# Performance work log

Hardware: AMD Instinct MI355X
Metric: run time of the kernel (lower is better)

## Reference

```python
import jax, jax.numpy as jnp
import numpy as np

EPS = 1e-5


def _layernorm(x, w, b):
    mu = jnp.mean(x, axis=-1, keepdims=True)
    var = jnp.var(x, axis=-1, keepdims=True)
    return (x - mu) * jax.lax.rsqrt(var + EPS) * w + b


def setup_inputs() -> dict:
    key = jax.random.key(0)
    ks = jax.random.split(key, 5)
    B, I, H = 8192, 1024, 1024
    inp = {
        "input": jax.random.normal(ks[0], (B, I), dtype=jnp.float32),
        "hx": jax.random.normal(ks[1], (B, H), dtype=jnp.float32),
        "cx": jax.random.normal(ks[2], (B, H), dtype=jnp.float32),
        # parameters (torch initializes weights with randn; LN weight=1, bias=0)
        "weight_ih": jax.random.normal(ks[3], (4 * H, I), dtype=jnp.float32),
        "weight_hh": jax.random.normal(ks[4], (4 * H, H), dtype=jnp.float32),
        "ln_i_w": jnp.ones((4 * H,), jnp.float32),
        "ln_i_b": jnp.zeros((4 * H,), jnp.float32),
        "ln_h_w": jnp.ones((4 * H,), jnp.float32),
        "ln_h_b": jnp.zeros((4 * H,), jnp.float32),
        "ln_c_w": jnp.ones((H,), jnp.float32),
        "ln_c_b": jnp.zeros((H,), jnp.float32),
    }
    return inp


def reference(input, hx, cx, weight_ih, weight_hh,
              ln_i_w, ln_i_b, ln_h_w, ln_h_b, ln_c_w, ln_c_b):
    # gate pre-activations: [B, 4H]
    igates = _layernorm(input @ weight_ih.T, ln_i_w, ln_i_b)
    hgates = _layernorm(hx @ weight_hh.T, ln_h_w, ln_h_b)
    gates = igates + hgates
    ingate, forgetgate, cellgate, outgate = jnp.split(gates, 4, axis=-1)
    ingate = jax.nn.sigmoid(ingate)
    forgetgate = jax.nn.sigmoid(forgetgate)
    cellgate = jnp.tanh(cellgate)
    outgate = jax.nn.sigmoid(outgate)
    cy = _layernorm(forgetgate * cx + ingate * cellgate, ln_c_w, ln_c_b)
    hy = outgate * jnp.tanh(cy)  # activation=Tanh, dropout p=0 is identity
    return (hy, cy)
```

## Files before the change

### kernel.cpp

```cpp
#include <hip/hip_runtime.h>
#include <hip/hip_bf16.h>
#include <cstdint>
#include <cstddef>

typedef __bf16 bf16_t;
typedef bf16_t bf16x8 __attribute__((ext_vector_type(8)));
typedef float floatx4 __attribute__((ext_vector_type(4)));

static constexpr int B_ = 8192;
static constexpr int H_ = 1024;
static constexpr int G4 = 4096;
static constexpr int K_ = 1024;

__device__ inline void async_copy16(const bf16_t* g, bf16_t* l) {
  auto l3 = (__attribute__((address_space(3))) void*)(uint32_t)(uintptr_t)l;
  __builtin_amdgcn_global_load_lds(
      (__attribute__((address_space(1))) void*)(uintptr_t)g, l3, 16, 0, 0);
}

__global__ __launch_bounds__(256) void prep_all(
    const float* __restrict__ input, const float* __restrict__ hx,
    const float* __restrict__ wih, const float* __restrict__ whh,
    bf16_t* __restrict__ Abf, bf16_t* __restrict__ Hbf,
    bf16_t* __restrict__ Wib, bf16_t* __restrict__ Whb) {
  const int bid = blockIdx.x;
  if (bid < 4096) {
    const int nt = B_ * K_ / 16;
    int gid = bid * 256 + threadIdx.x;
    const float* src; bf16_t* dst; int idx;
    if (gid < nt) { src = input; dst = Abf; idx = gid; }
    else          { src = hx;    dst = Hbf; idx = gid - nt; }
    const float4* s4 = (const float4*)src + (size_t)idx * 4;
    const float4 v0 = s4[0], v1 = s4[1], v2 = s4[2], v3 = s4[3];
    bf16x8 o0, o1;
    o0[0] = (bf16_t)v0.x; o0[1] = (bf16_t)v0.y; o0[2] = (bf16_t)v0.z; o0[3] = (bf16_t)v0.w;
    o0[4] = (bf16_t)v1.x; o0[5] = (bf16_t)v1.y; o0[6] = (bf16_t)v1.z; o0[7] = (bf16_t)v1.w;
    o1[0] = (bf16_t)v2.x; o1[1] = (bf16_t)v2.y; o1[2] = (bf16_t)v2.z; o1[3] = (bf16_t)v2.w;
    o1[4] = (bf16_t)v3.x; o1[5] = (bf16_t)v3.y; o1[6] = (bf16_t)v3.z; o1[7] = (bf16_t)v3.w;
    ((bf16x8*)dst)[(size_t)idx * 2]     = o0;
    ((bf16x8*)dst)[(size_t)idx * 2 + 1] = o1;
  } else {
    const int r  = bid - 4096;
    const int rr = r * 2 + (threadIdx.x >> 7);
    const int rp = rr & 4095;
    const float* src = (rr < 4096) ? wih : whh;
    bf16_t*      dst = (rr < 4096) ? Wib : Whb;
    const int h = rp >> 2, g = rp & 3;
    const int rin = g * 1024 + h;
    const int c = (threadIdx.x & 127) * 8;
    const float4 v0 = *(const float4*)(src + (size_t)rin * K_ + c);
    const float4 v1 = *(const float4*)(src + (size_t)rin * K_ + c + 4);
    bf16x8 o;
    o[0] = (bf16_t)v0.x; o[1] = (bf16_t)v0.y; o[2] = (bf16_t)v0.z; o[3] = (bf16_t)v0.w;
    o[4] = (bf16_t)v1.x; o[5] = (bf16_t)v1.y; o[6] = (bf16_t)v1.z; o[7] = (bf16_t)v1.w;
    *(bf16x8*)(dst + (size_t)rp * K_ + c) = o;
  }
}


#define FENCE() asm volatile("" ::: "memory")
#define BARRIER() do { FENCE(); __builtin_amdgcn_s_barrier(); FENCE(); } while (0)

__global__ __launch_bounds__(512, 2) void gemm_bt8(
    const bf16_t* __restrict__ A, const bf16_t* __restrict__ W,
    bf16_t* __restrict__ C) {
  constexpr int N = G4, K = K_, NT = K_ / 64;

  __shared__ bf16_t ldsA[2][16384];
  __shared__ bf16_t ldsB[2][16384];

  const int flatb = blockIdx.x + (blockIdx.y << 4);
  const int swzb  = (flatb & 7) * 64 + (flatb >> 3);
  const int by = swzb >> 4;
  const int bx = swzb & 15;

  const int tid  = threadIdx.x;
  const int lane = tid & 63;
  const int w    = tid >> 6;
  const int wm   = w >> 2, wn = w & 3;
  const int lrow = lane & 15, quad = lane >> 4;
  const int e    = lrow & 7;

  const int m0 = by * 256;
  const int n0 = bx * 256;

  const int srow   = tid >> 3;
  const int schunk = (tid & 7) ^ (srow & 7);
  const bf16_t* gA = A + (size_t)(m0 + srow) * K + schunk * 8;
  const bf16_t* gB = W + (size_t)(n0 + srow) * K + schunk * 8;
  const int wslot = w * 512;

  const int aBase = (wm * 128 + lrow) * 64 + (quad ^ e) * 8;
  const int bBase = (wn * 64 + lrow) * 64 + (quad ^ e) * 8;

  floatx4 acc[8][4] = {};
  bf16x8 aF[4][2];
  bf16x8 bF[2][2][2];

#define STG_A(p, half, kt) do {                                          \
    bf16_t* _l = &ldsA[p][(half) * 8192 + wslot];                        \
    async_copy16(gA + (size_t)((half) * 128) * K + (kt) * 64, _l);       \
    async_copy16(gA + (size_t)((half) * 128 + 64) * K + (kt) * 64, _l + 4096); \
  } while (0)
#define STG_B(p, half, kt) do {                                          \
    bf16_t* _l = &ldsB[p][(half) * 8192 + wslot];                        \
    async_copy16(gB + (size_t)((half) * 128) * K + (kt) * 64, _l);       \
    async_copy16(gB + (size_t)((half) * 128 + 64) * K + (kt) * 64, _l + 4096); \
  } while (0)

#define LD_A(p, qm) do { _Pragma("unroll")                               \
    for (int i2 = 0; i2 < 4; ++i2) {                                     \
      const int o = aBase + (qm) * 4096 + i2 * 1024;                     \
      aF[i2][0] = *(const bf16x8*)&ldsA[p][o];                           \
      aF[i2][1] = *(const bf16x8*)&ldsA[p][o ^ 32];                      \
    } } while (0)
#define LD_B(p, qn) do { _Pragma("unroll")                               \
    for (int j2 = 0; j2 < 2; ++j2) {                                     \
      const int o = bBase + (qn) * 2048 + j2 * 1024;                     \
      bF[qn][j2][0] = *(const bf16x8*)&ldsB[p][o];                       \
      bF[qn][j2][1] = *(const bf16x8*)&ldsB[p][o ^ 32];                  \
    } } while (0)
#define MFMA_Q(qm, qn) do { _Pragma("unroll")                            \
    for (int i2 = 0; i2 < 4; ++i2) { _Pragma("unroll")                   \
      for (int j2 = 0; j2 < 2; ++j2) {                                   \
        floatx4& c = acc[(qm) * 4 + i2][(qn) * 2 + j2];                  \
        c = __builtin_amdgcn_mfma_f32_16x16x32_bf16(aF[i2][0], bF[qn][j2][0], c, 0, 0, 0); \
        c = __builtin_amdgcn_mfma_f32_16x16x32_bf16(aF[i2][1], bF[qn][j2][1], c, 0, 0, 0); \
      } } } while (0)

  STG_B(0, 0, 0); STG_B(0, 1, 0);
  STG_A(0, 0, 0); STG_A(0, 1, 0);
  STG_B(1, 0, 1); STG_B(1, 1, 1);
  asm volatile("s_waitcnt vmcnt(4)" ::: "memory");
  BARRIER();

#pragma unroll 2
  for (int t = 0; t < NT; ++t) {
    const int p = t & 1, q = p ^ 1;
    const int t1 = (t + 1) & (NT - 1), t2 = (t + 2) & (NT - 1);

    LD_A(p, 0); LD_B(p, 0);
    STG_A(q, 0, t1);
    BARRIER();
    asm volatile("s_waitcnt lgkmcnt(0)" ::: "memory");
    __builtin_amdgcn_sched_barrier(0);
    __builtin_amdgcn_s_setprio(1); MFMA_Q(0, 0); __builtin_amdgcn_s_setprio(0);
    BARRIER();

    LD_B(p, 1);
    STG_A(q, 1, t1);
    BARRIER();
    asm volatile("s_waitcnt lgkmcnt(0)" ::: "memory");
    __builtin_amdgcn_sched_barrier(0);
    __builtin_amdgcn_s_setprio(1); MFMA_Q(0, 1); __builtin_amdgcn_s_setprio(0);
    BARRIER();

    LD_A(p, 1);
    STG_B(p, 0, t2);
    BARRIER();
    asm volatile("s_waitcnt lgkmcnt(0)" ::: "memory");
    __builtin_amdgcn_sched_barrier(0);
    __builtin_amdgcn_s_setprio(1); MFMA_Q(1, 0); __builtin_amdgcn_s_setprio(0);
    BARRIER();

    STG_B(p, 1, t2);
    BARRIER();
    __builtin_amdgcn_s_setprio(1); MFMA_Q(1, 1); __builtin_amdgcn_s_setprio(0);
    asm volatile("s_waitcnt vmcnt(4)" ::: "memory");
    BARRIER();
  }

#pragma unroll
  for (int i = 0; i < 8; ++i) {
    const int mbase = m0 + wm * 128 + i * 16 + quad * 4;
#pragma unroll
    for (int j = 0; j < 4; ++j) {
      const int n = n0 + wn * 64 + j * 16 + lrow;
#pragma unroll
      for (int r = 0; r < 4; ++r)
        C[(size_t)(mbase + r) * N + n] = (bf16_t)acc[i][j][r];
    }
  }
#undef STG_A
#undef STG_B
#undef LD_A
#undef LD_B
#undef MFMA_Q
}

__device__ inline float sigmoid_f(float x) { return 1.0f / (1.0f + __expf(-x)); }
__device__ inline float tanh_f(float x) {
  float e = __expf(2.0f * x);
  return 1.0f - 2.0f / (e + 1.0f);
}

__global__ __launch_bounds__(256) void ln_lstm_epi_wave2(
    const bf16_t* __restrict__ IG, const bf16_t* __restrict__ HG,
    const float* __restrict__ cx,
    const float* __restrict__ wi, const float* __restrict__ bi,
    const float* __restrict__ wh, const float* __restrict__ bh,
    const float* __restrict__ wc, const float* __restrict__ bc,
    float* __restrict__ hy_out, float* __restrict__ cy_out) {
  const int l = threadIdx.x & 63;
  const int b = blockIdx.x * 4 + (threadIdx.x >> 6);

  const bf16_t* igp = IG + (size_t)b * 4096;
  const bf16_t* hgp = HG + (size_t)b * 4096;

  bf16x8 igv[4][2], hgv[4][2];
  float4 cx4[4];
#pragma unroll
  for (int c = 0; c < 4; ++c) {
    const int n0 = c * 1024 + l * 16;
    igv[c][0] = *(const bf16x8*)(igp + n0);
    igv[c][1] = *(const bf16x8*)(igp + n0 + 8);
    hgv[c][0] = *(const bf16x8*)(hgp + n0);
    hgv[c][1] = *(const bf16x8*)(hgp + n0 + 8);
    cx4[c] = *(const float4*)(cx + (size_t)b * 1024 + c * 256 + l * 4);
  }

  float si = 0, qi = 0, sh = 0, qh = 0;
#pragma unroll
  for (int c = 0; c < 4; ++c)
#pragma unroll
    for (int hf = 0; hf < 2; ++hf)
#pragma unroll
      for (int e = 0; e < 8; ++e) {
        const float a = (float)igv[c][hf][e], d = (float)hgv[c][hf][e];
        si += a; qi = fmaf(a, a, qi);
        sh += d; qh = fmaf(d, d, qh);
      }
#pragma unroll
  for (int off = 1; off < 64; off <<= 1) {
    si += __shfl_xor(si, off); qi += __shfl_xor(qi, off);
    sh += __shfl_xor(sh, off); qh += __shfl_xor(qh, off);
  }
  const float invN = 1.0f / 4096.0f;
  const float mui = si * invN, muh = sh * invN;
  const float rsi = rsqrtf(fmaxf(qi * invN - mui * mui, 0.0f) + 1e-5f);
  const float rsh = rsqrtf(fmaxf(qh * invN - muh * muh, 0.0f) + 1e-5f);

  float cv[16], ov[16];
  float sc = 0, qc = 0;
#pragma unroll
  for (int c = 0; c < 4; ++c) {
    const int h0 = c * 256 + l * 4;
    float4 wiv[4], biv[4], whv[4], bhv[4];
#pragma unroll
    for (int g = 0; g < 4; ++g) {
      wiv[g] = *(const float4*)(wi + g * 1024 + h0);
      biv[g] = *(const float4*)(bi + g * 1024 + h0);
      whv[g] = *(const float4*)(wh + g * 1024 + h0);
      bhv[g] = *(const float4*)(bh + g * 1024 + h0);
    }
#pragma unroll
    for (int k = 0; k < 4; ++k) {
      float G[4];
#pragma unroll
      for (int g = 0; g < 4; ++g) {
        const int idx = k * 4 + g;
        const float gi = (float)igv[c][idx >> 3][idx & 7];
        const float gh = (float)hgv[c][idx >> 3][idx & 7];
        G[g] = (gi - mui) * rsi * ((const float*)&wiv[g])[k] + ((const float*)&biv[g])[k] +
               (gh - muh) * rsh * ((const float*)&whv[g])[k] + ((const float*)&bhv[g])[k];
      }
      const float in_g = sigmoid_f(G[0]);
      const float fo_g = sigmoid_f(G[1]);
      const float ce_g = tanh_f(G[2]);
      ov[c * 4 + k] = sigmoid_f(G[3]);
      const float cc = fo_g * ((const float*)&cx4[c])[k] + in_g * ce_g;
      cv[c * 4 + k] = cc;
      sc += cc; qc = fmaf(cc, cc, qc);
    }
  }
#pragma unroll
  for (int off = 1; off < 64; off <<= 1) {
    sc += __shfl_xor(sc, off); qc += __shfl_xor(qc, off);
  }
  const float invH = 1.0f / 1024.0f;
  const float muc = sc * invH;
  const float rsc = rsqrtf(fmaxf(qc * invH - muc * muc, 0.0f) + 1e-5f);

#pragma unroll
  for (int c = 0; c < 4; ++c) {
    const int h0 = c * 256 + l * 4;
    const float4 wc4 = *(const float4*)(wc + h0);
    const float4 bc4 = *(const float4*)(bc + h0);
    float4 cyv, hyv;
#pragma unroll
    for (int k = 0; k < 4; ++k) {
      const float cyn = (cv[c * 4 + k] - muc) * rsc * ((const float*)&wc4)[k] +
                        ((const float*)&bc4)[k];
      ((float*)&cyv)[k] = cyn;
      ((float*)&hyv)[k] = ov[c * 4 + k] * tanh_f(cyn);
    }
    *(float4*)(cy_out + (size_t)b * 1024 + h0) = cyv;
    *(float4*)(hy_out + (size_t)b * 1024 + h0) = hyv;
  }
}

extern "C" void kernel_launch(void* const* d_in, const int* in_sizes, int n_in,
                              void* d_out, int out_size, void* d_ws, size_t ws_size,
                              hipStream_t stream) {
  const float* input  = (const float*)d_in[0];
  const float* hx     = (const float*)d_in[1];
  const float* cx     = (const float*)d_in[2];
  const float* w_ih   = (const float*)d_in[3];
  const float* w_hh   = (const float*)d_in[4];
  const float* ln_i_w = (const float*)d_in[5];
  const float* ln_i_b = (const float*)d_in[6];
  const float* ln_h_w = (const float*)d_in[7];
  const float* ln_h_b = (const float*)d_in[8];
  const float* ln_c_w = (const float*)d_in[9];
  const float* ln_c_b = (const float*)d_in[10];

  float* out = (float*)d_out;
  float* hy = out;
  float* cy = out + (size_t)B_ * H_;

  bf16_t* Abf = (bf16_t*)d_ws;
  bf16_t* Hbf = Abf + (size_t)B_ * K_;
  bf16_t* Wib = Hbf + (size_t)B_ * K_;
  bf16_t* Whb = Wib + (size_t)G4 * K_;
  bf16_t* IG  = Whb + (size_t)G4 * K_;
  bf16_t* HG  = IG + (size_t)B_ * G4;

  prep_all<<<8192, 256, 0, stream>>>(input, hx, w_ih, w_hh, Abf, Hbf, Wib, Whb);

  gemm_bt8<<<dim3(16, 32), 512, 0, stream>>>(Abf, Wib, IG);
  gemm_bt8<<<dim3(16, 32), 512, 0, stream>>>(Hbf, Whb, HG);

  ln_lstm_epi_wave2<<<B_ / 4, 256, 0, stream>>>(IG, HG, cx, ln_i_w, ln_i_b,
                                                ln_h_w, ln_h_b, ln_c_w, ln_c_b, hy, cy);
}
```

Baseline: 372.5 us.

## Merge both gate GEMMs into one persistent kernel looping over four N tiles

Replaces the two separate 512-block GEMM launches with a single 256-workgroup kernel. Each workgroup handles one of the two GEMMs and iterates over four consecutive 256-wide N tiles, writing and resetting accumulators every 16 k-steps. The staging pipeline runs continuously across tile boundaries, prefetching the next tile's B. This is meant to remove a launch and the tail effects between the two GEMMs. The trade-off is one workgroup per CU, which halves the occupancy the launch bounds allow and may reduce latency hiding.

```diff
diff --git a/kernel.cpp b/kernel.cpp
--- a/kernel.cpp
+++ b/kernel.cpp
@@ -12,7 +12,7 @@
 static constexpr int G4 = 4096;
 static constexpr int K_ = 1024;
 
-__device__ inline void async_copy16(const bf16_t* g, bf16_t* l) {
+__device__ inline void async16(const void* g, void* l) {
   auto l3 = (__attribute__((address_space(3))) void*)(uint32_t)(uintptr_t)l;
   __builtin_amdgcn_global_load_lds(
       (__attribute__((address_space(1))) void*)(uintptr_t)g, l3, 16, 0, 0);
@@ -57,22 +57,27 @@
   }
 }
 
-
 #define FENCE() asm volatile("" ::: "memory")
 #define BARRIER() do { FENCE(); __builtin_amdgcn_s_barrier(); FENCE(); } while (0)
 
-__global__ __launch_bounds__(512, 2) void gemm_bt8(
-    const bf16_t* __restrict__ A, const bf16_t* __restrict__ W,
-    bf16_t* __restrict__ C) {
-  constexpr int N = G4, K = K_, NT = K_ / 64;
+__global__ __launch_bounds__(512, 2) void gemm_persist(
+    const bf16_t* __restrict__ A0, const bf16_t* __restrict__ A1,
+    const bf16_t* __restrict__ W0, const bf16_t* __restrict__ W1,
+    bf16_t* __restrict__ C0, bf16_t* __restrict__ C1) {
+  constexpr int N = G4, K = K_;
 
   __shared__ bf16_t ldsA[2][16384];
   __shared__ bf16_t ldsB[2][16384];
 
-  const int flatb = blockIdx.x + (blockIdx.y << 4);
-  const int swzb  = (flatb & 7) * 64 + (flatb >> 3);
-  const int by = swzb >> 4;
-  const int bx = swzb & 15;
+  const int k = blockIdx.x;
+  const int x = k & 7, s = k >> 3;
+  const int z   = x >> 2;
+  const int by  = (x & 3) * 8 + (s >> 2);
+  const int bxb = (s & 3) * 4;
+
+  const bf16_t* A = z ? A1 : A0;
+  const bf16_t* W = z ? W1 : W0;
+  bf16_t*       C = z ? C1 : C0;
 
   const int tid  = threadIdx.x;
   const int lane = tid & 63;
@@ -81,13 +86,13 @@
   const int lrow = lane & 15, quad = lane >> 4;
   const int e    = lrow & 7;
 
-  const int m0 = by * 256;
-  const int n0 = bx * 256;
+  const int m0  = by * 256;
+  const int n0b = bxb * 256;
 
   const int srow   = tid >> 3;
   const int schunk = (tid & 7) ^ (srow & 7);
   const bf16_t* gA = A + (size_t)(m0 + srow) * K + schunk * 8;
-  const bf16_t* gB = W + (size_t)(n0 + srow) * K + schunk * 8;
+  const bf16_t* gB = W + (size_t)(n0b + srow) * K + schunk * 8;
   const int wslot = w * 512;
 
   const int aBase = (wm * 128 + lrow) * 64 + (quad ^ e) * 8;
@@ -99,13 +104,14 @@
 
 #define STG_A(p, half, kt) do {                                          \
     bf16_t* _l = &ldsA[p][(half) * 8192 + wslot];                        \
-    async_copy16(gA + (size_t)((half) * 128) * K + (kt) * 64, _l);       \
-    async_copy16(gA + (size_t)((half) * 128 + 64) * K + (kt) * 64, _l + 4096); \
+    async16(gA + (size_t)((half) * 128) * K + (kt) * 64, _l);            \
+    async16(gA + (size_t)((half) * 128 + 64) * K + (kt) * 64, _l + 4096); \
   } while (0)
-#define STG_B(p, half, kt) do {                                          \
+#define STG_B(p, half, jb, kt) do {                                      \
     bf16_t* _l = &ldsB[p][(half) * 8192 + wslot];                        \
-    async_copy16(gB + (size_t)((half) * 128) * K + (kt) * 64, _l);       \
-    async_copy16(gB + (size_t)((half) * 128 + 64) * K + (kt) * 64, _l + 4096); \
+    const bf16_t* _g = gB + (size_t)((jb) * 256 + (half) * 128) * K + (kt) * 64; \
+    async16(_g, _l);                                                     \
+    async16(_g + (size_t)64 * K, _l + 4096);                             \
   } while (0)
 
 #define LD_A(p, qm) do { _Pragma("unroll")                               \
@@ -128,19 +134,22 @@
         c = __builtin_amdgcn_mfma_f32_16x16x32_bf16(aF[i2][1], bF[qn][j2][1], c, 0, 0, 0); \
       } } } while (0)
 
-  STG_B(0, 0, 0); STG_B(0, 1, 0);
-  STG_A(0, 0, 0); STG_A(0, 1, 0);
-  STG_B(1, 0, 1); STG_B(1, 1, 1);
+  STG_B(0, 0, 0, 0); STG_B(0, 1, 0, 0);
+  STG_A(0, 0, 0);    STG_A(0, 1, 0);
+  STG_B(1, 0, 0, 1); STG_B(1, 1, 0, 1);
   asm volatile("s_waitcnt vmcnt(4)" ::: "memory");
   BARRIER();
 
 #pragma unroll 2
-  for (int t = 0; t < NT; ++t) {
-    const int p = t & 1, q = p ^ 1;
-    const int t1 = (t + 1) & (NT - 1), t2 = (t + 2) & (NT - 1);
+  for (int T = 0; T < 64; ++T) {
+    const int p = T & 1, q = p ^ 1;
+    const int Ta = (T + 1) & 63;
+    const int Tb = (T + 2) & 63;
+    const int kta = Ta & 15;
+    const int jbb = Tb >> 4, ktb = Tb & 15;
 
     LD_A(p, 0); LD_B(p, 0);
-    STG_A(q, 0, t1);
+    STG_A(q, 0, kta);
     BARRIER();
     asm volatile("s_waitcnt lgkmcnt(0)" ::: "memory");
     __builtin_amdgcn_sched_barrier(0);
@@ -148,7 +157,7 @@
     BARRIER();
 
     LD_B(p, 1);
-    STG_A(q, 1, t1);
+    STG_A(q, 1, kta);
     BARRIER();
     asm volatile("s_waitcnt lgkmcnt(0)" ::: "memory");
     __builtin_amdgcn_sched_barrier(0);
@@ -156,29 +165,37 @@
     BARRIER();
 
     LD_A(p, 1);
-    STG_B(p, 0, t2);
+    STG_B(p, 0, jbb, ktb);
     BARRIER();
     asm volatile("s_waitcnt lgkmcnt(0)" ::: "memory");
     __builtin_amdgcn_sched_barrier(0);
     __builtin_amdgcn_s_setprio(1); MFMA_Q(1, 0); __builtin_amdgcn_s_setprio(0);
     BARRIER();
 
-    STG_B(p, 1, t2);
+    STG_B(p, 1, jbb, ktb);
     BARRIER();
     __builtin_amdgcn_s_setprio(1); MFMA_Q(1, 1); __builtin_amdgcn_s_setprio(0);
     asm volatile("s_waitcnt vmcnt(4)" ::: "memory");
     BARRIER();
-  }
-
-#pragma unroll
-  for (int i = 0; i < 8; ++i) {
-    const int mbase = m0 + wm * 128 + i * 16 + quad * 4;
-#pragma unroll
-    for (int j = 0; j < 4; ++j) {
-      const int n = n0 + wn * 64 + j * 16 + lrow;
-#pragma unroll
-      for (int r = 0; r < 4; ++r)
-        C[(size_t)(mbase + r) * N + n] = (bf16_t)acc[i][j][r];
+
+    if ((T & 15) == 15) {
+      const int n0 = n0b + (T >> 4) * 256;
+#pragma unroll
+      for (int i = 0; i < 8; ++i) {
+        const int mbase = m0 + wm * 128 + i * 16 + quad * 4;
+#pragma unroll
+        for (int j = 0; j < 4; ++j) {
+          const int n = n0 + wn * 64 + j * 16 + lrow;
+#pragma unroll
+          for (int r = 0; r < 4; ++r)
+            C[(size_t)(mbase + r) * N + n] = (bf16_t)acc[i][j][r];
+        }
+      }
+#pragma unroll
+      for (int i = 0; i < 8; ++i)
+#pragma unroll
+        for (int j = 0; j < 4; ++j)
+          acc[i][j] = floatx4{0.f, 0.f, 0.f, 0.f};
     }
   }
 #undef STG_A
@@ -254,22 +271,22 @@
       bhv[g] = *(const float4*)(bh + g * 1024 + h0);
     }
 #pragma unroll
-    for (int k = 0; k < 4; ++k) {
+    for (int kk = 0; kk < 4; ++kk) {
       float G[4];
 #pragma unroll
       for (int g = 0; g < 4; ++g) {
-        const int idx = k * 4 + g;
+        const int idx = kk * 4 + g;
         const float gi = (float)igv[c][idx >> 3][idx & 7];
         const float gh = (float)hgv[c][idx >> 3][idx & 7];
-        G[g] = (gi - mui) * rsi * ((const float*)&wiv[g])[k] + ((const float*)&biv[g])[k] +
-               (gh - muh) * rsh * ((const float*)&whv[g])[k] + ((const float*)&bhv[g])[k];
+        G[g] = (gi - mui) * rsi * ((const float*)&wiv[g])[kk] + ((const float*)&biv[g])[kk] +
+               (gh - muh) * rsh * ((const float*)&whv[g])[kk] + ((const float*)&bhv[g])[kk];
       }
       const float in_g = sigmoid_f(G[0]);
       const float fo_g = sigmoid_f(G[1]);
       const float ce_g = tanh_f(G[2]);
-      ov[c * 4 + k] = sigmoid_f(G[3]);
-      const float cc = fo_g * ((const float*)&cx4[c])[k] + in_g * ce_g;
-      cv[c * 4 + k] = cc;
+      ov[c * 4 + kk] = sigmoid_f(G[3]);
+      const float cc = fo_g * ((const float*)&cx4[c])[kk] + in_g * ce_g;
+      cv[c * 4 + kk] = cc;
       sc += cc; qc = fmaf(cc, cc, qc);
     }
   }
@@ -288,11 +305,11 @@
     const float4 bc4 = *(const float4*)(bc + h0);
     float4 cyv, hyv;
 #pragma unroll
-    for (int k = 0; k < 4; ++k) {
-      const float cyn = (cv[c * 4 + k] - muc) * rsc * ((const float*)&wc4)[k] +
-                        ((const float*)&bc4)[k];
-      ((float*)&cyv)[k] = cyn;
-      ((float*)&hyv)[k] = ov[c * 4 + k] * tanh_f(cyn);
+    for (int kk = 0; kk < 4; ++kk) {
+      const float cyn = (cv[c * 4 + kk] - muc) * rsc * ((const float*)&wc4)[kk] +
+                        ((const float*)&bc4)[kk];
+      ((float*)&cyv)[kk] = cyn;
+      ((float*)&hyv)[kk] = ov[c * 4 + kk] * tanh_f(cyn);
     }
     *(float4*)(cy_out + (size_t)b * 1024 + h0) = cyv;
     *(float4*)(hy_out + (size_t)b * 1024 + h0) = hyv;
@@ -327,9 +344,8 @@
 
   prep_all<<<8192, 256, 0, stream>>>(input, hx, w_ih, w_hh, Abf, Hbf, Wib, Whb);
 
-  gemm_bt8<<<dim3(16, 32), 512, 0, stream>>>(Abf, Wib, IG);
-  gemm_bt8<<<dim3(16, 32), 512, 0, stream>>>(Hbf, Whb, HG);
-
-  ln_lstm_epi_wave2<<<B_ / 4, 256, 0, stream>>>(IG, HG, cx, ln_i_w, ln_i_b,
-                                                ln_h_w, ln_h_b, ln_c_w, ln_c_b, hy, cy);
-}
+  gemm_persist<<<256, 512, 0, stream>>>(Abf, Hbf, Wib, Whb, IG, HG);
+
+  ln_lstm_epi_wave2<<<2048, 256, 0, stream>>>(IG, HG, cx, ln_i_w, ln_i_b,
+                                              ln_h_w, ln_h_b, ln_c_w, ln_c_b, hy, cy);
+}
```

New measurement: 369.4 us. Within noise of the previous version (-0.9%).
